# Optimization experiments

Hardware: AMD Instinct MI355X
Metric: run time of the kernel (lower is better)

Reference implementation:

```python
import jax, jax.numpy as jnp
import numpy as np

EMBED, HEADS, WIN, UP = 180, 6, 16, 4
HDIM = EMBED // HEADS

def _win_part(x, ws):
    # x: [B, H, W, C] -> [B*(H//ws)*(W//ws), ws, ws, C]
    B, H, W, C = x.shape
    x = x.reshape(B, H // ws, ws, W // ws, ws, C).transpose(0, 1, 3, 2, 4, 5)
    return x.reshape(-1, ws, ws, C)

def _win_rev(w, ws, H, W):
    # inverse of _win_part
    C = w.shape[-1]
    B = w.shape[0] // ((H // ws) * (W // ws))
    x = w.reshape(B, H // ws, W // ws, ws, ws, C).transpose(0, 1, 3, 2, 4, 5)
    return x.reshape(B, H, W, C)

def _ln(x, g, b):
    mu = x.mean(-1, keepdims=True)
    v = ((x - mu) ** 2).mean(-1, keepdims=True)
    return (x - mu) * jax.lax.rsqrt(v + 1e-5) * g + b

def _forward(gumbel_u, x, sel1_w, sel1_b, sel2_w, sel2_b, sel3_w, sel3_b,
             embed_w, embed_b, ln1_g, ln1_b, qkv_w, qkv_b, proj_w, proj_b,
             ln2_g, ln2_b, mlp1_w, mlp1_b, mlp2_w, mlp2_b, up_w, up_b):
    B, C, H, W = x.shape
    ws = H // 4                                     # 64 -> 16 tiles per image
    tiles = _win_part(x.transpose(0, 2, 3, 1), ws)  # [T, ws, ws, C]
    T = tiles.shape[0]
    # --- TileSelection (pooled MLP router) ---
    pooled = tiles.reshape(T, 8, ws // 8, 8, ws // 8, C).mean((2, 4)).reshape(T, 8 * 8 * C)
    f1 = pooled @ sel1_w + sel1_b
    f2 = jax.nn.relu(f1) @ sel2_w + sel2_b
    f3 = jax.nn.relu(f2) @ sel3_w + sel3_b          # [T, 2] routing logits
    # --- hard gumbel-softmax with straight-through estimator (tau=1) ---
    g = -jnp.log(-jnp.log(gumbel_u + 1e-10) + 1e-10)
    y_soft = jax.nn.softmax(f3 + g, axis=-1)
    y_hard = jax.nn.one_hot(jnp.argmax(y_soft, -1), 2, dtype=y_soft.dtype)
    pi = jax.lax.stop_gradient(y_hard - y_soft) + y_soft
    mask = pi[:, 1]                                 # 1 -> transformer expert
    # --- TR expert (SwinIR-style block, dense dispatch over all tiles) ---
    tok = tiles.reshape(T, ws * ws, C) @ embed_w + embed_b   # [T, 4096, 180]
    h = _ln(tok, ln1_g, ln1_b)
    hw = _win_part(h.reshape(T, ws, ws, EMBED), WIN).reshape(-1, WIN * WIN, EMBED)
    Nw, L = hw.shape[0], WIN * WIN
    qkv = (hw @ qkv_w + qkv_b).reshape(Nw, L, 3, HEADS, HDIM)
    q, k, v = qkv[:, :, 0], qkv[:, :, 1], qkv[:, :, 2]
    attn = jax.nn.softmax(jnp.einsum('nlhd,nmhd->nhlm', q, k) / np.sqrt(HDIM).astype(np.float32), axis=-1)
    av = jnp.einsum('nhlm,nmhd->nlhd', attn, v).reshape(Nw, L, EMBED)
    av = av @ proj_w + proj_b
    av = _win_rev(av.reshape(Nw, WIN, WIN, EMBED), WIN, ws, ws).reshape(T, ws * ws, EMBED)
    tok = tok + av
    h2 = _ln(tok, ln2_g, ln2_b)
    tok = tok + jax.nn.gelu(h2 @ mlp1_w + mlp1_b) @ mlp2_w + mlp2_b
    # pixelshuffle x4 upsample: 180 -> 3*4*4
    up = (tok @ up_w + up_b).reshape(T, ws, ws, UP, UP, C)
    up = up.transpose(0, 1, 3, 2, 4, 5).reshape(T, ws * UP, ws * UP, C)
    # --- cheap expert: bicubic x4 ---
    neg = jax.image.resize(tiles, (T, ws * UP, ws * UP, C), method='bicubic')
    # --- combine per-tile and reassemble ---
    m = mask[:, None, None, None]
    sr_tiles = m * up + (1.0 - m) * neg             # [T, 4ws, 4ws, C]
    sr = _win_rev(sr_tiles, H, H * UP, W * UP)      # [B, 4H, 4W, C]
    return sr.transpose(0, 3, 1, 2), f3, f2, f1

def setup_inputs() -> dict:
    key = jax.random.key(0)
    ks = jax.random.split(key, 16)
    B, C, H, W = 1, 3, 256, 256
    T = B * 16
    p = lambda k, s: jax.random.normal(k, s, jnp.float32) * 0.02
    return {
        'x': jax.random.normal(ks[0], (B, C, H, W), jnp.float32),
        'gumbel_u': jax.random.uniform(ks[1], (T, 2), jnp.float32),
        'sel1_w': p(ks[2], (192, 64)), 'sel1_b': jnp.zeros((64,), jnp.float32),
        'sel2_w': p(ks[3], (64, 32)), 'sel2_b': jnp.zeros((32,), jnp.float32),
        'sel3_w': p(ks[4], (32, 2)), 'sel3_b': jnp.zeros((2,), jnp.float32),
        'embed_w': p(ks[5], (3, EMBED)), 'embed_b': jnp.zeros((EMBED,), jnp.float32),
        'ln1_g': jnp.ones((EMBED,), jnp.float32), 'ln1_b': jnp.zeros((EMBED,), jnp.float32),
        'qkv_w': p(ks[6], (EMBED, 3 * EMBED)), 'qkv_b': jnp.zeros((3 * EMBED,), jnp.float32),
        'proj_w': p(ks[7], (EMBED, EMBED)), 'proj_b': jnp.zeros((EMBED,), jnp.float32),
        'ln2_g': jnp.ones((EMBED,), jnp.float32), 'ln2_b': jnp.zeros((EMBED,), jnp.float32),
        'mlp1_w': p(ks[8], (EMBED, 2 * EMBED)), 'mlp1_b': jnp.zeros((2 * EMBED,), jnp.float32),
        'mlp2_w': p(ks[9], (2 * EMBED, EMBED)), 'mlp2_b': jnp.zeros((EMBED,), jnp.float32),
        'up_w': p(ks[10], (EMBED, 3 * UP * UP)), 'up_b': jnp.zeros((3 * UP * UP,), jnp.float32),
    }

def reference(x, gumbel_u, sel1_w, sel1_b, sel2_w, sel2_b, sel3_w, sel3_b,
              embed_w, embed_b, ln1_g, ln1_b, qkv_w, qkv_b, proj_w, proj_b,
              ln2_g, ln2_b, mlp1_w, mlp1_b, mlp2_w, mlp2_b, up_w, up_b):
    return _forward(gumbel_u, x, sel1_w, sel1_b, sel2_w, sel2_b, sel3_w, sel3_b,
                    embed_w, embed_b, ln1_g, ln1_b, qkv_w, qkv_b, proj_w, proj_b,
                    ln2_g, ln2_b, mlp1_w, mlp1_b, mlp2_w, mlp2_b, up_w, up_b)
```

## Files before the change

kernel.cpp:

```cpp
#include <hip/hip_runtime.h>
#include <hip/hip_bf16.h>
#include <cstdint>

typedef __hip_bfloat16 bf16;
typedef __attribute__((ext_vector_type(8))) short short8;
typedef __attribute__((ext_vector_type(4))) short short4v;
typedef __attribute__((ext_vector_type(4))) float f32x4;
typedef __attribute__((ext_vector_type(2))) unsigned int uint2v;

__device__ __forceinline__ float bf2f(bf16 v) { return __bfloat162float(v); }
__device__ __forceinline__ bf16  f2bf(float v) { return __float2bfloat16(v); }
__device__ __forceinline__ float rbf(short s) {
  union { uint32_t u; float f; } c; c.u = ((uint32_t)(uint16_t)s) << 16; return c.f;
}
__device__ __forceinline__ short wbf(float f) {
  bf16 h = f2bf(f); return *(short*)&h;
}
__device__ __forceinline__ uint32_t pack2(float a, float b) {
  bf16 x = f2bf(a), y = f2bf(b);
  return (uint32_t)(*(uint16_t*)&x) | ((uint32_t)(*(uint16_t*)&y) << 16);
}
__device__ __forceinline__ uint2v pack4(float a, float b, float c, float d) {
  uint2v r; r[0] = pack2(a, b); r[1] = pack2(c, d); return r;
}
__device__ __forceinline__ int swz(int row, int g) { return g ^ (row & 7); }

__device__ __forceinline__ int win_to_token(int m) {
  int n = m >> 8, l = m & 255;
  int t = n >> 4, win = n & 15;
  int wi = win >> 2, wj = win & 3;
  int u = l >> 4, v = l & 15;
  return (t << 12) | ((wi * 16 + u) << 6) | (wj * 16 + v);
}

__global__ __launch_bounds__(256) void k_packsel(
    const float* __restrict__ qkvw, const float* __restrict__ projw,
    const float* __restrict__ mlp1w, const float* __restrict__ mlp2w,
    const float* __restrict__ upw, const float* __restrict__ qkvb,
    bf16* __restrict__ Bt_qkv, bf16* __restrict__ Bt_proj,
    bf16* __restrict__ Bt_mlp1, bf16* __restrict__ Bt_mlp2,
    bf16* __restrict__ Bt_up, float* __restrict__ biasq,
    const float* __restrict__ x, const float* __restrict__ gu,
    const float* __restrict__ s1w, const float* __restrict__ s1b,
    const float* __restrict__ s2w, const float* __restrict__ s2b,
    const float* __restrict__ s3w, const float* __restrict__ s3b,
    float* __restrict__ f1o, float* __restrict__ f2o, float* __restrict__ f3o,
    float* __restrict__ maskp) {
  if (blockIdx.x < 1203) {
    int idx = blockIdx.x * 256 + threadIdx.x;
    const int e0 = 576 * 192, e1 = e0 + 192 * 192, e2 = e1 + 384 * 192,
              e3 = e2 + 192 * 384, e4 = e3 + 64 * 192, e5 = e4 + 576;
    if (idx < e0) {
      int np = idx / 192, k = idx % 192;
      int buf = np / 192, colp = np % 192;
      int hd = colp >> 5, dd = colp & 31;
      float v = 0.f;
      if (dd < 30 && k < 180) v = qkvw[(size_t)k * 540 + buf * 180 + hd * 30 + dd];
      Bt_qkv[idx] = f2bf(v);
    } else if (idx < e1) {
      int off = idx - e0; int n = off / 192, kp = off % 192;
      int hd = kp >> 5, dd = kp & 31;
      float v = (dd < 30 && n < 180) ? projw[(size_t)(hd * 30 + dd) * 180 + n] : 0.f;
      Bt_proj[off] = f2bf(v);
    } else if (idx < e2) {
      int off = idx - e1; int n = off / 192, k = off % 192;
      Bt_mlp1[off] = f2bf((k < 180 && n < 360) ? mlp1w[(size_t)k * 360 + n] : 0.f);
    } else if (idx < e3) {
      int off = idx - e2; int n = off / 384, k = off % 384;
      Bt_mlp2[off] = f2bf((k < 360 && n < 180) ? mlp2w[(size_t)k * 180 + n] : 0.f);
    } else if (idx < e4) {
      int off = idx - e3; int n = off / 192, k = off % 192;
      Bt_up[off] = f2bf((k < 180 && n < 48) ? upw[(size_t)k * 48 + n] : 0.f);
    } else if (idx < e5) {
      int np = idx - e4;
      int buf = np / 192, colp = np % 192;
      int hd = colp >> 5, dd = colp & 31;
      biasq[np] = (dd < 30) ? qkvb[buf * 180 + hd * 30 + dd] : 0.f;
    }
    return;
  }
  int t = blockIdx.x - 1203;
  int tid = threadIdx.x;
  int th = t >> 2, tw = t & 3;
  __shared__ float pooled[192];
  __shared__ float red[256];
  __shared__ float f1s[64], f2s[32], f3s[2];
  if (tid < 192) {
    int ch = tid % 3, j = (tid / 3) & 7, i = tid / 24;
    const float* xp = x + ch * 65536 + (th * 64 + i * 8) * 256 + (tw * 64 + j * 8);
    float s = 0.f;
#pragma unroll
    for (int a = 0; a < 8; ++a)
#pragma unroll
      for (int b = 0; b < 8; ++b) s += xp[a * 256 + b];
    pooled[tid] = s * (1.0f / 64.0f);
  }
  __syncthreads();
  {
    int o = tid & 63, part = tid >> 6;
    float s = 0.f;
    for (int k = part * 48; k < part * 48 + 48; ++k) s = fmaf(pooled[k], s1w[k * 64 + o], s);
    red[tid] = s;
  }
  __syncthreads();
  if (tid < 64) {
    float v = red[tid] + red[tid + 64] + red[tid + 128] + red[tid + 192] + s1b[tid];
    f1o[t * 64 + tid] = v;
    f1s[tid] = fmaxf(v, 0.f);
  }
  __syncthreads();
  {
    int o = tid & 31, part = tid >> 5;
    float s = 0.f;
    for (int k = part * 8; k < part * 8 + 8; ++k) s = fmaf(f1s[k], s2w[k * 32 + o], s);
    red[tid] = s;
  }
  __syncthreads();
  if (tid < 32) {
    float v = s2b[tid];
#pragma unroll
    for (int p = 0; p < 8; ++p) v += red[tid + p * 32];
    f2o[t * 32 + tid] = v;
    f2s[tid] = fmaxf(v, 0.f);
  }
  __syncthreads();
  if (tid < 2) {
    float s = s3b[tid];
    for (int k = 0; k < 32; ++k) s = fmaf(f2s[k], s3w[k * 2 + tid], s);
    f3o[t * 2 + tid] = s;
    f3s[tid] = s;
  }
  __syncthreads();
  if (tid == 0) {
    float g0 = -logf(-logf(gu[t * 2 + 0] + 1e-10f) + 1e-10f);
    float g1 = -logf(-logf(gu[t * 2 + 1] + 1e-10f) + 1e-10f);
    maskp[t] = (f3s[1] + g1 > f3s[0] + g0) ? 1.0f : 0.0f;
  }
}

__global__ __launch_bounds__(256) void k_embed(
    const float* __restrict__ x, const float* __restrict__ ew,
    const float* __restrict__ eb, const float* __restrict__ g1,
    const float* __restrict__ b1, bf16* __restrict__ tok,
    bf16* __restrict__ Aq) {
  int wrow = blockIdx.x * 4 + (threadIdx.x >> 6);
  int lane = threadIdx.x & 63;
  int token = win_to_token(wrow);
  int t = token >> 12, p = token & 4095;
  int r = p >> 6, c = p & 63;
  int gh = (t >> 2) * 64 + r, gw = (t & 3) * 64 + c;
  float x0 = x[gh * 256 + gw];
  float x1 = x[65536 + gh * 256 + gw];
  float x2 = x[131072 + gh * 256 + gw];
  float v[3];
  float s = 0.f, s2 = 0.f;
#pragma unroll
  for (int i = 0; i < 3; ++i) {
    int e = lane + i * 64;
    float vv = 0.f;
    if (e < 180) {
      vv = eb[e];
      vv = fmaf(x0, ew[e], vv);
      vv = fmaf(x1, ew[180 + e], vv);
      vv = fmaf(x2, ew[360 + e], vv);
      tok[(size_t)wrow * 180 + e] = f2bf(vv);
      s += vv; s2 = fmaf(vv, vv, s2);
    }
    v[i] = vv;
  }
#pragma unroll
  for (int off = 32; off; off >>= 1) { s += __shfl_xor(s, off); s2 += __shfl_xor(s2, off); }
  float mu = s * (1.f / 180.f);
  float rs = rsqrtf(s2 * (1.f / 180.f) - mu * mu + 1e-5f);
#pragma unroll
  for (int i = 0; i < 3; ++i) {
    int e = lane + i * 64;
    if (e < 192) {
      float a = (e < 180) ? ((v[i] - mu) * rs * g1[e] + b1[e]) : 0.f;
      Aq[(size_t)wrow * 192 + e] = f2bf(a);
    }
  }
}

__global__ __launch_bounds__(512, 2) void k_qkv3(
    const bf16* __restrict__ A, const bf16* __restrict__ Bt,
    const float* __restrict__ biasq, bf16* __restrict__ Qp,
    bf16* __restrict__ Kp, bf16* __restrict__ Vp) {
  __shared__ bf16 Bs[2][64 * 192];
  const int tid = threadIdx.x;
  const int w = tid >> 6, l = tid & 63;
  const int lr = l & 15, lk = l >> 4;
  const int row = blockIdx.x * 128 + w * 16 + lr;

  short8 fa[6];
  {
    const bf16* Ab = A + (size_t)row * 192 + lk * 8;
#pragma unroll
    for (int ks = 0; ks < 6; ++ks) fa[ks] = *(const short8*)(Ab + ks * 32);
  }

  for (int c = tid; c < 1536; c += 512) {
    int n = c / 24, g = c % 24;
    *(short8*)&Bs[0][n * 192 + swz(n, g) * 8] = *(const short8*)(Bt + (size_t)n * 192 + g * 8);
  }

  for (int nt = 0; nt < 9; ++nt) {
    __syncthreads();
    if (nt < 8) {
      const bf16* src = Bt + (size_t)(nt + 1) * 64 * 192;
      bf16* dstb = Bs[(nt + 1) & 1];
      for (int c = tid; c < 1536; c += 512) {
        int n = c / 24, g = c % 24;
        *(short8*)&dstb[n * 192 + swz(n, g) * 8] = *(const short8*)(src + (size_t)n * 192 + g * 8);
      }
    }
    const bf16* Bb = Bs[nt & 1];
    f32x4 acc[4];
#pragma unroll
    for (int j = 0; j < 4; ++j) acc[j] = (f32x4){0.f, 0.f, 0.f, 0.f};
#pragma unroll
    for (int ks = 0; ks < 6; ++ks) {
      short8 fb[4];
#pragma unroll
      for (int j = 0; j < 4; ++j) {
        int rn = j * 16 + lr;
        fb[j] = *(const short8*)&Bb[rn * 192 + swz(rn, ks * 4 + lk) * 8];
      }
#pragma unroll
      for (int j = 0; j < 4; ++j)
        acc[j] = __builtin_amdgcn_mfma_f32_16x16x32_bf16(fb[j], fa[ks], acc[j], 0, 0, 0);
    }
    bf16* dst = (nt < 3) ? Qp : (nt < 6) ? Kp : Vp;
    int c0 = (nt % 3) * 64;
#pragma unroll
    for (int j = 0; j < 4; ++j) {
      int np = nt * 64 + j * 16 + lk * 4;
      f32x4 bv = *(const f32x4*)&biasq[np];
      *(uint2v*)(dst + (size_t)row * 192 + c0 + j * 16 + lk * 4) =
          pack4(acc[j][0] + bv[0], acc[j][1] + bv[1], acc[j][2] + bv[2], acc[j][3] + bv[3]);
    }
  }
}

__global__ __launch_bounds__(256) void k_attn2(
    const bf16* __restrict__ Qp, const bf16* __restrict__ Kp,
    const bf16* __restrict__ Vp, bf16* __restrict__ av) {
  const int blk = blockIdx.x;
  const int win = blk / 6, hd = blk % 6;
  const int tid = threadIdx.x;
  const int w = tid >> 6, l = tid & 63;
  const int lr = l & 15, lk = l >> 4;
  const float scale = 0.18257418583505536f;

  __shared__ bf16 Ks[256][40];
  __shared__ bf16 Vs[32][264];
  __shared__ bf16 Ps[4][16][264];

  {
    const bf16* src = Kp + (size_t)(win * 256 + tid) * 192 + hd * 32;
#pragma unroll
    for (int c = 0; c < 4; ++c)
      *(short8*)&Ks[tid][c * 8] = *(const short8*)(src + c * 8);
  }
  {
    const bf16* src = Vp + (size_t)(win * 256 + tid) * 192 + hd * 32;
    short8 vv[4];
#pragma unroll
    for (int c = 0; c < 4; ++c) vv[c] = *(const short8*)(src + c * 8);
#pragma unroll
    for (int c = 0; c < 4; ++c)
#pragma unroll
      for (int e = 0; e < 8; ++e)
        *(short*)&Vs[c * 8 + e][tid] = vv[c][e];
  }
  __syncthreads();

  for (int qt = 0; qt < 4; ++qt) {
    const int qbase = qt * 64 + w * 16;
    short8 fq = *(const short8*)(Qp + (size_t)(win * 256 + qbase + lr) * 192 + hd * 32 + lk * 8);
    f32x4 accS[16];
#pragma unroll
    for (int kt = 0; kt < 16; ++kt) {
      short8 fk = *(const short8*)(&Ks[kt * 16 + lr][lk * 8]);
      accS[kt] = __builtin_amdgcn_mfma_f32_16x16x32_bf16(
          fk, fq, (f32x4){0.f, 0.f, 0.f, 0.f}, 0, 0, 0);
    }
    float mraw = -1e30f;
#pragma unroll
    for (int kt = 0; kt < 16; ++kt)
#pragma unroll
      for (int r = 0; r < 4; ++r) mraw = fmaxf(mraw, accS[kt][r]);
    mraw = fmaxf(mraw, __shfl_xor(mraw, 16));
    mraw = fmaxf(mraw, __shfl_xor(mraw, 32));
    const float mc = mraw * scale;
    float lsum = 0.f;
#pragma unroll
    for (int kt = 0; kt < 16; ++kt) {
      float p0 = __expf(fmaf(accS[kt][0], scale, -mc));
      float p1 = __expf(fmaf(accS[kt][1], scale, -mc));
      float p2 = __expf(fmaf(accS[kt][2], scale, -mc));
      float p3 = __expf(fmaf(accS[kt][3], scale, -mc));
      lsum += (p0 + p1) + (p2 + p3);
      *(uint32_t*)&Ps[w][lr][kt * 16 + lk * 4]     = pack2(p0, p1);
      *(uint32_t*)&Ps[w][lr][kt * 16 + lk * 4 + 2] = pack2(p2, p3);
    }
    lsum += __shfl_xor(lsum, 16);
    lsum += __shfl_xor(lsum, 32);
    __syncthreads();
    f32x4 accO0 = (f32x4){0.f, 0.f, 0.f, 0.f};
    f32x4 accO1 = (f32x4){0.f, 0.f, 0.f, 0.f};
#pragma unroll
    for (int ks = 0; ks < 8; ++ks) {
      short8 fp  = *(const short8*)(&Ps[w][lr][ks * 32 + lk * 8]);
      short8 fv0 = *(const short8*)(&Vs[lr][ks * 32 + lk * 8]);
      short8 fv1 = *(const short8*)(&Vs[16 + lr][ks * 32 + lk * 8]);
      accO0 = __builtin_amdgcn_mfma_f32_16x16x32_bf16(fv0, fp, accO0, 0, 0, 0);
      accO1 = __builtin_amdgcn_mfma_f32_16x16x32_bf16(fv1, fp, accO1, 0, 0, 0);
    }
    float invl = 1.f / lsum;
    bf16* avrow = av + (size_t)(win * 256 + qbase + lr) * 192 + hd * 32;
    *(uint2v*)(avrow + lk * 4) =
        pack4(accO0[0] * invl, accO0[1] * invl, accO0[2] * invl, accO0[3] * invl);
    *(uint2v*)(avrow + 16 + lk * 4) =
        pack4(accO1[0] * invl, accO1[1] * invl, accO1[2] * invl, accO1[3] * invl);
    __syncthreads();
  }
}

__global__ __launch_bounds__(512, 2) void k_post(
    const bf16* __restrict__ av, const bf16* __restrict__ tok,
    const bf16* __restrict__ Btp, const float* __restrict__ pb,
    const float* __restrict__ g2, const float* __restrict__ b2,
    const bf16* __restrict__ Bt1, const float* __restrict__ b1m,
    const bf16* __restrict__ Bt2, const float* __restrict__ b2m,
    const bf16* __restrict__ Btu, const float* __restrict__ bu,
    bf16* __restrict__ up) {
  __shared__ bf16 Bs[2][64 * 192];
  __shared__ bf16 Hmid[128 * 64];
  const int tid = threadIdx.x;
  const int w = tid >> 6, l = tid & 63;
  const int lr = l & 15, lk = l >> 4;
  const int row_l = w * 16 + lr;
  const int row_g = blockIdx.x * 128 + row_l;
  const int half = (lk & 1) * 4;
  const int sa = lr + 32 * (lk & 1);
  const int sb = sa + 16;
  const bool hi2 = (lk >= 2);

#define STAGE_A(srcp, dstb)                                               \
  {                                                                       \
    const bf16* _s = (srcp);                                              \
    bf16* _d = (dstb);                                                    \
    for (int c = tid; c < 1536; c += 512) {                               \
      int n = c / 24, g = c % 24;                                         \
      *(short8*)&_d[n * 192 + swz(n, g) * 8] =                            \
          *(const short8*)(_s + (size_t)n * 192 + g * 8);                 \
    }                                                                     \
  }
#define STAGE_S(ntv, dstb)                                                \
  {                                                                       \
    bf16* _d = (dstb);                                                    \
    for (int c = tid; c < 1536; c += 512) {                               \
      int n = c / 8, g = c % 8;                                           \
      *(short8*)&_d[n * 64 + swz(n, g) * 8] =                             \
          *(const short8*)(Bt2 + (size_t)n * 384 + (ntv) * 64 + g * 8);   \
    }                                                                     \
  }
#define GATHER_FH(dstf, pk, ksv)                                          \
  {                                                                       \
    const int _nt = (ksv) >> 1, _jA = ((ksv) & 1) * 2, _jB = _jA + 1;     \
    uint32_t _a0 = (uint32_t)__shfl((int)pk[_nt][_jA][0], sa);            \
    uint32_t _a1 = (uint32_t)__shfl((int)pk[_nt][_jA][1], sa);            \
    uint32_t _b0 = (uint32_t)__shfl((int)pk[_nt][_jB][0], sa);            \
    uint32_t _b1 = (uint32_t)__shfl((int)pk[_nt][_jB][1], sa);            \
    uint32_t _c0 = (uint32_t)__shfl((int)pk[_nt][_jA][0], sb);            \
    uint32_t _c1 = (uint32_t)__shfl((int)pk[_nt][_jA][1], sb);            \
    uint32_t _d0 = (uint32_t)__shfl((int)pk[_nt][_jB][0], sb);            \
    uint32_t _d1 = (uint32_t)__shfl((int)pk[_nt][_jB][1], sb);            \
    uint32_t _t[4];                                                       \
    _t[0] = hi2 ? _b0 : _a0;                                              \
    _t[1] = hi2 ? _b1 : _a1;                                              \
    _t[2] = hi2 ? _d0 : _c0;                                              \
    _t[3] = hi2 ? _d1 : _c1;                                              \
    __builtin_memcpy(&(dstf), _t, 16);                                    \
  }

  short8 fa[6];
  {
    const bf16* ab = av + (size_t)row_g * 192 + lk * 8;
#pragma unroll
    for (int ks = 0; ks < 6; ++ks) fa[ks] = *(const short8*)(ab + ks * 32);
  }

  short4v t2p[3][4];
  float sA = 0.f, s2A = 0.f;

  STAGE_A(Btp, Bs[0]);

#pragma unroll
  for (int nt = 0; nt < 3; ++nt) {
    __syncthreads();
    if (nt < 2) { STAGE_A(Btp + (size_t)(nt + 1) * 64 * 192, Bs[(nt + 1) & 1]); }
    else        { STAGE_A(Bt1, Bs[1]); }
    const bf16* Bb = Bs[nt & 1];
    f32x4 acc[4];
#pragma unroll
    for (int j = 0; j < 4; ++j) acc[j] = (f32x4){0.f, 0.f, 0.f, 0.f};
#pragma unroll
    for (int ks = 0; ks < 6; ++ks) {
      short8 fb[4];
#pragma unroll
      for (int j = 0; j < 4; ++j) {
        int rn = j * 16 + lr;
        fb[j] = *(const short8*)&Bb[rn * 192 + swz(rn, ks * 4 + lk) * 8];
      }
#pragma unroll
      for (int j = 0; j < 4; ++j)
        acc[j] = __builtin_amdgcn_mfma_f32_16x16x32_bf16(fb[j], fa[ks], acc[j], 0, 0, 0);
    }
#pragma unroll
    for (int j = 0; j < 4; ++j) {
      int n = nt * 64 + j * 16 + lk * 4;
      if (n < 180) {
        f32x4 bv = *(const f32x4*)&pb[n];
        short4v tv = *(const short4v*)(tok + (size_t)row_g * 180 + n);
#pragma unroll
        for (int q = 0; q < 4; ++q) {
          float v = acc[j][q] + bv[q] + rbf(tv[q]);
          sA += v; s2A = fmaf(v, v, s2A);
          t2p[nt][j][q] = wbf(v);
        }
      } else {
#pragma unroll
        for (int q = 0; q < 4; ++q) t2p[nt][j][q] = 0;
      }
    }
  }

  short8 fh[6];
  {
    sA += __shfl_xor(sA, 16);  sA += __shfl_xor(sA, 32);
    s2A += __shfl_xor(s2A, 16); s2A += __shfl_xor(s2A, 32);
    float mu = sA * (1.f / 180.f);
    float rs = rsqrtf(s2A * (1.f / 180.f) - mu * mu + 1e-5f);
    uint2v hpk[3][4];
#pragma unroll
    for (int nt = 0; nt < 3; ++nt)
#pragma unroll
      for (int j = 0; j < 4; ++j) {
        int n = nt * 64 + j * 16 + lk * 4;
        float h[4] = {0.f, 0.f, 0.f, 0.f};
        if (n < 180) {
          f32x4 gv = *(const f32x4*)&g2[n];
          f32x4 bv = *(const f32x4*)&b2[n];
#pragma unroll
          for (int q = 0; q < 4; ++q)
            h[q] = (rbf(t2p[nt][j][q]) - mu) * rs * gv[q] + bv[q];
        }
        hpk[nt][j] = pack4(h[0], h[1], h[2], h[3]);
      }
#pragma unroll
    for (int ks = 0; ks < 6; ++ks) GATHER_FH(fh[ks], hpk, ks);
  }

  f32x4 acc2[3][4];
#pragma unroll
  for (int t = 0; t < 3; ++t)
#pragma unroll
    for (int j = 0; j < 4; ++j) acc2[t][j] = (f32x4){0.f, 0.f, 0.f, 0.f};

#pragma unroll
  for (int nt = 0; nt < 6; ++nt) {
    __syncthreads();
    STAGE_S(nt, Bs[0]);
    {
      const bf16* Bb = Bs[1];
      f32x4 acc1[4];
#pragma unroll
      for (int j = 0; j < 4; ++j) acc1[j] = (f32x4){0.f, 0.f, 0.f, 0.f};
#pragma unroll
      for (int ks = 0; ks < 6; ++ks) {
        short8 fb[4];
#pragma unroll
        for (int j = 0; j < 4; ++j) {
          int rn = j * 16 + lr;
          fb[j] = *(const short8*)&Bb[rn * 192 + swz(rn, ks * 4 + lk) * 8];
        }
#pragma unroll
        for (int j = 0; j < 4; ++j)
          acc1[j] = __builtin_amdgcn_mfma_f32_16x16x32_bf16(fb[j], fh[ks], acc1[j], 0, 0, 0);
      }
#pragma unroll
      for (int j = 0; j < 4; ++j) {
        int n = nt * 64 + j * 16 + lk * 4;
        float m4[4] = {0.f, 0.f, 0.f, 0.f};
        if (n < 360) {
          f32x4 bv = *(const f32x4*)&b1m[n];
#pragma unroll
          for (int q = 0; q < 4; ++q) {
            float v = acc1[j][q] + bv[q];
            float u = 0.7978845608028654f * (v + 0.044715f * v * v * v);
            m4[q] = v / (1.f + __expf(-2.f * u));
          }
        }
        int g = j * 2 + (lk >> 1);
        *(uint2v*)&Hmid[row_l * 64 + swz(row_l, g) * 8 + half] = pack4(m4[0], m4[1], m4[2], m4[3]);
      }
    }
    __syncthreads();
    if (nt < 5) { STAGE_A(Bt1 + (size_t)(nt + 1) * 64 * 192, Bs[1]); }
    else        { STAGE_A(Btu, Bs[1]); }
    {
      short8 fm[2];
#pragma unroll
      for (int s = 0; s < 2; ++s)
        fm[s] = *(const short8*)&Hmid[row_l * 64 + swz(row_l, s * 4 + lk) * 8];
#pragma unroll
      for (int s = 0; s < 2; ++s)
#pragma unroll
        for (int t = 0; t < 3; ++t)
#pragma unroll
          for (int j = 0; j < 4; ++j) {
            int rn = t * 64 + j * 16 + lr;
            short8 fb2 = *(const short8*)&Bs[0][rn * 64 + swz(rn, s * 4 + lk) * 8];
            acc2[t][j] = __builtin_amdgcn_mfma_f32_16x16x32_bf16(fb2, fm[s], acc2[t][j], 0, 0, 0);
          }
    }
  }

  __syncthreads();
  short8 ft[6];
  {
    uint2v tpk[3][4];
#pragma unroll
    for (int t = 0; t < 3; ++t)
#pragma unroll
      for (int j = 0; j < 4; ++j) {
        int n = t * 64 + j * 16 + lk * 4;
        float o4[4] = {0.f, 0.f, 0.f, 0.f};
        if (n < 180) {
          f32x4 bv = *(const f32x4*)&b2m[n];
#pragma unroll
          for (int q = 0; q < 4; ++q) o4[q] = acc2[t][j][q] + bv[q] + rbf(t2p[t][j][q]);
        }
        tpk[t][j] = pack4(o4[0], o4[1], o4[2], o4[3]);
      }
#pragma unroll
    for (int ks = 0; ks < 6; ++ks) GATHER_FH(ft[ks], tpk, ks);
  }

  f32x4 acc3[3];
#pragma unroll
  for (int j = 0; j < 3; ++j) acc3[j] = (f32x4){0.f, 0.f, 0.f, 0.f};
#pragma unroll
  for (int ks = 0; ks < 6; ++ks) {
    short8 fb[3];
#pragma unroll
    for (int j = 0; j < 3; ++j) {
      int rn = j * 16 + lr;
      fb[j] = *(const short8*)&Bs[1][rn * 192 + swz(rn, ks * 4 + lk) * 8];
    }
#pragma unroll
    for (int j = 0; j < 3; ++j)
      acc3[j] = __builtin_amdgcn_mfma_f32_16x16x32_bf16(fb[j], ft[ks], acc3[j], 0, 0, 0);
  }
#pragma unroll
  for (int j = 0; j < 3; ++j) {
    int n = j * 16 + lk * 4;
    f32x4 bv = *(const f32x4*)&bu[n];
    *(uint2v*)(up + (size_t)row_g * 48 + n) =
        pack4(acc3[j][0] + bv[0], acc3[j][1] + bv[1], acc3[j][2] + bv[2], acc3[j][3] + bv[3]);
  }
#undef STAGE_A
#undef STAGE_S
#undef GATHER_FH
}

__device__ const float c_cubw[4][4] = {
    {-0.0439453125f, 0.3896484375f, 0.7275390625f, -0.0732421875f},
    {-0.0068359375f, 0.0908203125f, 0.9638671875f, -0.0478515625f},
    {-0.0478515625f, 0.9638671875f, 0.0908203125f, -0.0068359375f},
    {-0.0732421875f, 0.7275390625f, 0.3896484375f, -0.0439453125f},
};

__device__ __forceinline__ void cubw(int r, int ph, float* w, int& base) {
  base = r + ((ph < 2) ? -2 : -1);
  float sum = 0.f;
#pragma unroll
  for (int i = 0; i < 4; ++i) {
    int idx = base + i;
    float wi = (idx >= 0 && idx < 64) ? c_cubw[ph][i] : 0.f;
    w[i] = wi; sum += wi;
  }
  float inv = 1.f / sum;
#pragma unroll
  for (int i = 0; i < 4; ++i) w[i] *= inv;
}

__global__ __launch_bounds__(256) void k_blend(
    const bf16* __restrict__ up, const float* __restrict__ x,
    const float* __restrict__ maskp, float* __restrict__ sr) {
  int idx = blockIdx.x * 256 + threadIdx.x;
  int ch = idx >> 20;
  int rem = idx & 1048575;
  int gR = rem >> 10, gC = rem & 1023;
  int th = gR >> 8, tw = gC >> 8;
  int t = th * 4 + tw;
  int R = gR & 255, C = gC & 255;
  int r = R >> 2, a = R & 3, c = C >> 2, b = C & 3;
  float m = maskp[t];
  float outv;
  if (m > 0.5f) {
    int wi = r >> 4, u = r & 15, wj = c >> 4, v = c & 15;
    int wrow = (t * 16 + wi * 4 + wj) * 256 + u * 16 + v;
    outv = bf2f(up[(size_t)wrow * 48 + a * 12 + b * 3 + ch]);
  } else {
    float wy[4], wx[4];
    int yb, xb;
    cubw(r, a, wy, yb);
    cubw(c, b, wx, xb);
    const float* xc = x + ch * 65536;
    float neg = 0.f;
#pragma unroll
    for (int i = 0; i < 4; ++i) {
      int yi = yb + i;
      if (yi < 0 || yi > 63) continue;
      float rowsum = 0.f;
#pragma unroll
      for (int j = 0; j < 4; ++j) {
        int xj = xb + j;
        if (xj < 0 || xj > 63) continue;
        rowsum = fmaf(wx[j], xc[(th * 64 + yi) * 256 + tw * 64 + xj], rowsum);
      }
      neg = fmaf(wy[i], rowsum, neg);
    }
    outv = neg;
  }
  sr[idx] = outv;
}

extern "C" void kernel_launch(void* const* d_in, const int* in_sizes, int n_in,
                              void* d_out, int out_size, void* d_ws, size_t ws_size,
                              hipStream_t stream) {
  const float* x     = (const float*)d_in[0];
  const float* gu    = (const float*)d_in[1];
  const float* s1w   = (const float*)d_in[2];
  const float* s1b   = (const float*)d_in[3];
  const float* s2w   = (const float*)d_in[4];
  const float* s2b   = (const float*)d_in[5];
  const float* s3w   = (const float*)d_in[6];
  const float* s3b   = (const float*)d_in[7];
  const float* ew    = (const float*)d_in[8];
  const float* ebias = (const float*)d_in[9];
  const float* ln1g  = (const float*)d_in[10];
  const float* ln1b  = (const float*)d_in[11];
  const float* qkvw  = (const float*)d_in[12];
  const float* qkvb  = (const float*)d_in[13];
  const float* projw = (const float*)d_in[14];
  const float* projb = (const float*)d_in[15];
  const float* ln2g  = (const float*)d_in[16];
  const float* ln2b  = (const float*)d_in[17];
  const float* mlp1w = (const float*)d_in[18];
  const float* mlp1b = (const float*)d_in[19];
  const float* mlp2w = (const float*)d_in[20];
  const float* mlp2b = (const float*)d_in[21];
  const float* upw   = (const float*)d_in[22];
  const float* upb   = (const float*)d_in[23];

  float* out = (float*)d_out;
  float* sr  = out;
  float* f3o = out + 3145728;
  float* f2o = f3o + 32;
  float* f1o = f2o + 512;

  char* ws = (char*)d_ws;
  bf16* tok  = (bf16*)(ws);
  bf16* ABuf = (bf16*)(ws + 23592960);
  bf16* Qp   = (bf16*)(ws + 48758784);
  bf16* Kp   = (bf16*)(ws + 73924608);
  bf16* Vp   = (bf16*)(ws + 99090432);
  float* maskp   = (float*)(ws + 124256256);
  bf16* Bt_qkv  = (bf16*)(ws + 124256320);
  bf16* Bt_proj = (bf16*)(ws + 124477504);
  bf16* Bt_mlp1 = (bf16*)(ws + 124551232);
  bf16* Bt_mlp2 = (bf16*)(ws + 124698688);
  bf16* Bt_up   = (bf16*)(ws + 124846144);
  float* biasq  = (float*)(ws + 124870720);
  bf16* up      = (bf16*)(ws + 124873088);
  bf16* av = ABuf;

  k_packsel<<<1219, 256, 0, stream>>>(qkvw, projw, mlp1w, mlp2w, upw, qkvb,
                                      Bt_qkv, Bt_proj, Bt_mlp1, Bt_mlp2, Bt_up, biasq,
                                      x, gu, s1w, s1b, s2w, s2b, s3w, s3b,
                                      f1o, f2o, f3o, maskp);
  k_embed<<<16384, 256, 0, stream>>>(x, ew, ebias, ln1g, ln1b, tok, ABuf);
  k_qkv3<<<512, 512, 0, stream>>>(ABuf, Bt_qkv, biasq, Qp, Kp, Vp);
  k_attn2<<<1536, 256, 0, stream>>>(Qp, Kp, Vp, av);
  k_post<<<512, 512, 0, stream>>>(av, tok, Bt_proj, projb, ln2g, ln2b,
                                  Bt_mlp1, mlp1b, Bt_mlp2, mlp2b, Bt_up, upb, up);
  k_blend<<<12288, 256, 0, stream>>>(up, x, maskp, sr);
}
```

Baseline: 204.9 us.

## Fuse LayerNorm1 into QKV GEMM prologue and drop attention barriers

The embed kernel now writes only the padded 192-wide token buffer, and LayerNorm1 moves into the QKV GEMM's A-fragment load, with per-row stats reduced by lane shuffles and padded gamma/beta packed in the setup kernel. This removes one full write and read of the normalized activation buffer (about 25 MB of bf16). The two __syncthreads in the attention loop are also removed, which is only safe if no shared memory is reused across those points. The token stride changes from 180 to 192, so k_post's residual read is updated to match.

Result: slower. 228.7 us (+11.6%).

```diff
diff --git a/kernel.cpp b/kernel.cpp
--- a/kernel.cpp
+++ b/kernel.cpp
@@ -37,19 +37,22 @@
     const float* __restrict__ qkvw, const float* __restrict__ projw,
     const float* __restrict__ mlp1w, const float* __restrict__ mlp2w,
     const float* __restrict__ upw, const float* __restrict__ qkvb,
+    const float* __restrict__ ln1g, const float* __restrict__ ln1b,
     bf16* __restrict__ Bt_qkv, bf16* __restrict__ Bt_proj,
     bf16* __restrict__ Bt_mlp1, bf16* __restrict__ Bt_mlp2,
     bf16* __restrict__ Bt_up, float* __restrict__ biasq,
+    float* __restrict__ g1p, float* __restrict__ b1p,
     const float* __restrict__ x, const float* __restrict__ gu,
     const float* __restrict__ s1w, const float* __restrict__ s1b,
     const float* __restrict__ s2w, const float* __restrict__ s2b,
     const float* __restrict__ s3w, const float* __restrict__ s3b,
     float* __restrict__ f1o, float* __restrict__ f2o, float* __restrict__ f3o,
     float* __restrict__ maskp) {
-  if (blockIdx.x < 1203) {
+  if (blockIdx.x < 1204) {
     int idx = blockIdx.x * 256 + threadIdx.x;
     const int e0 = 576 * 192, e1 = e0 + 192 * 192, e2 = e1 + 384 * 192,
-              e3 = e2 + 192 * 384, e4 = e3 + 64 * 192, e5 = e4 + 576;
+              e3 = e2 + 192 * 384, e4 = e3 + 64 * 192, e5 = e4 + 576,
+              e6 = e5 + 192, e7 = e6 + 192;
     if (idx < e0) {
       int np = idx / 192, k = idx % 192;
       int buf = np / 192, colp = np % 192;
@@ -76,10 +79,16 @@
       int buf = np / 192, colp = np % 192;
       int hd = colp >> 5, dd = colp & 31;
       biasq[np] = (dd < 30) ? qkvb[buf * 180 + hd * 30 + dd] : 0.f;
+    } else if (idx < e6) {
+      int e = idx - e5;
+      g1p[e] = (e < 180) ? ln1g[e] : 0.f;
+    } else if (idx < e7) {
+      int e = idx - e6;
+      b1p[e] = (e < 180) ? ln1b[e] : 0.f;
     }
     return;
   }
-  int t = blockIdx.x - 1203;
+  int t = blockIdx.x - 1204;
   int tid = threadIdx.x;
   int th = t >> 2, tw = t & 3;
   __shared__ float pooled[192];
@@ -140,9 +149,7 @@
 
 __global__ __launch_bounds__(256) void k_embed(
     const float* __restrict__ x, const float* __restrict__ ew,
-    const float* __restrict__ eb, const float* __restrict__ g1,
-    const float* __restrict__ b1, bf16* __restrict__ tok,
-    bf16* __restrict__ Aq) {
+    const float* __restrict__ eb, bf16* __restrict__ tok) {
   int wrow = blockIdx.x * 4 + (threadIdx.x >> 6);
   int lane = threadIdx.x & 63;
   int token = win_to_token(wrow);
@@ -152,8 +159,6 @@
   float x0 = x[gh * 256 + gw];
   float x1 = x[65536 + gh * 256 + gw];
   float x2 = x[131072 + gh * 256 + gw];
-  float v[3];
-  float s = 0.f, s2 = 0.f;
 #pragma unroll
   for (int i = 0; i < 3; ++i) {
     int e = lane + i * 64;
@@ -163,28 +168,15 @@
       vv = fmaf(x0, ew[e], vv);
       vv = fmaf(x1, ew[180 + e], vv);
       vv = fmaf(x2, ew[360 + e], vv);
-      tok[(size_t)wrow * 180 + e] = f2bf(vv);
-      s += vv; s2 = fmaf(vv, vv, s2);
-    }
-    v[i] = vv;
-  }
-#pragma unroll
-  for (int off = 32; off; off >>= 1) { s += __shfl_xor(s, off); s2 += __shfl_xor(s2, off); }
-  float mu = s * (1.f / 180.f);
-  float rs = rsqrtf(s2 * (1.f / 180.f) - mu * mu + 1e-5f);
-#pragma unroll
-  for (int i = 0; i < 3; ++i) {
-    int e = lane + i * 64;
-    if (e < 192) {
-      float a = (e < 180) ? ((v[i] - mu) * rs * g1[e] + b1[e]) : 0.f;
-      Aq[(size_t)wrow * 192 + e] = f2bf(a);
-    }
+    }
+    tok[(size_t)wrow * 192 + e] = f2bf(vv);
   }
 }
 
 __global__ __launch_bounds__(512, 2) void k_qkv3(
-    const bf16* __restrict__ A, const bf16* __restrict__ Bt,
-    const float* __restrict__ biasq, bf16* __restrict__ Qp,
+    const bf16* __restrict__ tok, const bf16* __restrict__ Bt,
+    const float* __restrict__ biasq, const float* __restrict__ g1p,
+    const float* __restrict__ b1p, bf16* __restrict__ Qp,
     bf16* __restrict__ Kp, bf16* __restrict__ Vp) {
   __shared__ bf16 Bs[2][64 * 192];
   const int tid = threadIdx.x;
@@ -194,9 +186,32 @@
 
   short8 fa[6];
   {
-    const bf16* Ab = A + (size_t)row * 192 + lk * 8;
-#pragma unroll
-    for (int ks = 0; ks < 6; ++ks) fa[ks] = *(const short8*)(Ab + ks * 32);
+    const bf16* Ab = tok + (size_t)row * 192 + lk * 8;
+    float s = 0.f, s2 = 0.f;
+#pragma unroll
+    for (int ks = 0; ks < 6; ++ks) {
+      fa[ks] = *(const short8*)(Ab + ks * 32);
+#pragma unroll
+      for (int e = 0; e < 8; ++e) { float v = rbf(fa[ks][e]); s += v; s2 = fmaf(v, v, s2); }
+    }
+    s += __shfl_xor(s, 16);  s += __shfl_xor(s, 32);
+    s2 += __shfl_xor(s2, 16); s2 += __shfl_xor(s2, 32);
+    float mu = s * (1.f / 180.f);
+    float rs = rsqrtf(s2 * (1.f / 180.f) - mu * mu + 1e-5f);
+#pragma unroll
+    for (int ks = 0; ks < 6; ++ks) {
+      int kb = ks * 32 + lk * 8;
+      f32x4 gv0 = *(const f32x4*)&g1p[kb];
+      f32x4 gv1 = *(const f32x4*)&g1p[kb + 4];
+      f32x4 bv0 = *(const f32x4*)&b1p[kb];
+      f32x4 bv1 = *(const f32x4*)&b1p[kb + 4];
+      short8 o;
+#pragma unroll
+      for (int e = 0; e < 4; ++e) o[e] = wbf((rbf(fa[ks][e]) - mu) * rs * gv0[e] + bv0[e]);
+#pragma unroll
+      for (int e = 0; e < 4; ++e) o[4 + e] = wbf((rbf(fa[ks][4 + e]) - mu) * rs * gv1[e] + bv1[e]);
+      fa[ks] = o;
+    }
   }
 
   for (int c = tid; c < 1536; c += 512) {
@@ -306,7 +321,6 @@
     }
     lsum += __shfl_xor(lsum, 16);
     lsum += __shfl_xor(lsum, 32);
-    __syncthreads();
     f32x4 accO0 = (f32x4){0.f, 0.f, 0.f, 0.f};
     f32x4 accO1 = (f32x4){0.f, 0.f, 0.f, 0.f};
 #pragma unroll
@@ -323,7 +337,6 @@
         pack4(accO0[0] * invl, accO0[1] * invl, accO0[2] * invl, accO0[3] * invl);
     *(uint2v*)(avrow + 16 + lk * 4) =
         pack4(accO1[0] * invl, accO1[1] * invl, accO1[2] * invl, accO1[3] * invl);
-    __syncthreads();
   }
 }
 
@@ -423,7 +436,7 @@
       int n = nt * 64 + j * 16 + lk * 4;
       if (n < 180) {
         f32x4 bv = *(const f32x4*)&pb[n];
-        short4v tv = *(const short4v*)(tok + (size_t)row_g * 180 + n);
+        short4v tv = *(const short4v*)(tok + (size_t)row_g * 192 + n);
 #pragma unroll
         for (int q = 0; q < 4; ++q) {
           float v = acc[j][q] + bv[q] + rbf(tv[q]);
@@ -675,26 +688,29 @@
 
   char* ws = (char*)d_ws;
   bf16* tok  = (bf16*)(ws);
-  bf16* ABuf = (bf16*)(ws + 23592960);
-  bf16* Qp   = (bf16*)(ws + 48758784);
-  bf16* Kp   = (bf16*)(ws + 73924608);
-  bf16* Vp   = (bf16*)(ws + 99090432);
-  float* maskp   = (float*)(ws + 124256256);
-  bf16* Bt_qkv  = (bf16*)(ws + 124256320);
-  bf16* Bt_proj = (bf16*)(ws + 124477504);
-  bf16* Bt_mlp1 = (bf16*)(ws + 124551232);
-  bf16* Bt_mlp2 = (bf16*)(ws + 124698688);
-  bf16* Bt_up   = (bf16*)(ws + 124846144);
-  float* biasq  = (float*)(ws + 124870720);
-  bf16* up      = (bf16*)(ws + 124873088);
+  bf16* ABuf = (bf16*)(ws + 25165824);
+  bf16* Qp   = (bf16*)(ws + 50331648);
+  bf16* Kp   = (bf16*)(ws + 75497472);
+  bf16* Vp   = (bf16*)(ws + 100663296);
+  float* maskp   = (float*)(ws + 125829120);
+  bf16* Bt_qkv  = (bf16*)(ws + 125829184);
+  bf16* Bt_proj = (bf16*)(ws + 126050368);
+  bf16* Bt_mlp1 = (bf16*)(ws + 126124096);
+  bf16* Bt_mlp2 = (bf16*)(ws + 126271552);
+  bf16* Bt_up   = (bf16*)(ws + 126419008);
+  float* biasq  = (float*)(ws + 126443584);
+  float* g1p    = (float*)(ws + 126445888);
+  float* b1p    = (float*)(ws + 126446656);
+  bf16* up      = (bf16*)(ws + 126447424);
   bf16* av = ABuf;
 
-  k_packsel<<<1219, 256, 0, stream>>>(qkvw, projw, mlp1w, mlp2w, upw, qkvb,
+  k_packsel<<<1220, 256, 0, stream>>>(qkvw, projw, mlp1w, mlp2w, upw, qkvb, ln1g, ln1b,
                                       Bt_qkv, Bt_proj, Bt_mlp1, Bt_mlp2, Bt_up, biasq,
+                                      g1p, b1p,
                                       x, gu, s1w, s1b, s2w, s2b, s3w, s3b,
                                       f1o, f2o, f3o, maskp);
-  k_embed<<<16384, 256, 0, stream>>>(x, ew, ebias, ln1g, ln1b, tok, ABuf);
-  k_qkv3<<<512, 512, 0, stream>>>(ABuf, Bt_qkv, biasq, Qp, Kp, Vp);
+  k_embed<<<16384, 256, 0, stream>>>(x, ew, ebias, tok);
+  k_qkv3<<<512, 512, 0, stream>>>(tok, Bt_qkv, biasq, g1p, b1p, Qp, Kp, Vp);
   k_attn2<<<1536, 256, 0, stream>>>(Qp, Kp, Vp, av);
   k_post<<<512, 512, 0, stream>>>(av, tok, Bt_proj, projb, ln2g, ln2b,
                                   Bt_mlp1, mlp1b, Bt_mlp2, mlp2b, Bt_up, upb, up);
```
